# Performance work log

Measured on AMD Instinct MI355X. Metric: run time of the kernel, lower is better.

Reference implementation:

```python
import jax, jax.numpy as jnp
import numpy as np

N, F_IN, HID, OUT, K, L = 16000, 16, 256, 128, 8, 3


def setup_inputs() -> dict:
    key = jax.random.key(0)
    ks = jax.random.split(key, 8)
    rn = lambda k, sh, sc: (jax.random.normal(k, sh, jnp.float32) * sc)
    return {
        "x": rn(ks[0], (N, F_IN), 1.0),
        "coords": rn(ks[1], (N, 3), 1.0),
        "We": rn(ks[2], (F_IN, HID), 0.1),
        "be": jnp.zeros((HID,), jnp.float32),
        "gnn_W": rn(ks[3], (L, HID, HID), 0.05),
        "gnn_b": jnp.zeros((L, HID), jnp.float32),
        "Wp1": rn(ks[4], (HID, HID // 2), 0.05),
        "bp1": jnp.zeros((HID // 2,), jnp.float32),
        "Wp2": rn(ks[5], (HID // 2, OUT), 0.05),
        "bp2": jnp.zeros((OUT,), jnp.float32),
    }


def knn_edges(coords, k=K):
    # squared pairwise distances (same ordering as torch.cdist) -> kNN, drop self
    sq = jnp.sum(coords * coords, axis=1)
    d2 = sq[:, None] + sq[None, :] - 2.0 * (coords @ coords.T)  # [N, N]
    _, idx = jax.lax.top_k(-d2, k + 1)            # smallest k+1 (incl. self)
    nbr = idx[:, 1:]                               # [N, k]
    src = jnp.broadcast_to(jnp.arange(coords.shape[0])[:, None], nbr.shape)
    return src.reshape(-1), nbr.reshape(-1)       # edge_index rows


def gcn_layer(h, W, b, src, dst, n):
    # GCN with added self-loops and symmetric degree normalization
    deg = jnp.ones((n,), h.dtype).at[dst].add(1.0)   # in-degree + self-loop
    norm = jax.lax.rsqrt(deg)
    hw = h @ W                                        # [N, HID]
    msg = hw[src] * (norm[src] * norm[dst])[:, None]  # gather + scale
    agg = jax.ops.segment_sum(msg, dst, num_segments=n)
    agg = agg + hw * (norm * norm)[:, None]           # self-loop term
    return agg + b


def reference(x, coords, We, be, gnn_W, gnn_b, Wp1, bp1, Wp2, bp2):
    n = x.shape[0]
    src, dst = knn_edges(coords)
    h = x @ We + be                     # survey encoder -> [N, HID]
    for i in range(L):
        h = gcn_layer(h, gnn_W[i], gnn_b[i], src, dst, n)
        h = jax.nn.relu(h)              # dropout is identity in eval mode
    g = jnp.mean(h, axis=0)             # mean pooling (batch=None) -> [HID]
    out = jax.nn.relu(g @ Wp1 + bp1) @ Wp2 + bp2  # output projection -> [OUT]
    return out
```

## Files before the change

### kernel.cpp

```cpp
#include <hip/hip_runtime.h>
#include <math.h>

#define N_NODES 16000
#define F_IN    16
#define HID     256
#define OUTD    128
#define KNN     8
#define LAYERS  3
#define NEDGE   (N_NODES * KNN)

#define NPAD    16384
#define PARTS   4
#define PART_SZ (NPAD / PARTS)
#define SEGS    32
#define NMIN    (PARTS * SEGS)
#define CAPP    32
#define NZERO   32256

typedef __attribute__((ext_vector_type(8))) short  s8v;
typedef __attribute__((ext_vector_type(4))) float  f4v;

__device__ __forceinline__ unsigned short f2bf(float x) {
    unsigned u = __float_as_uint(x);
    unsigned r = u + 0x7fffu + ((u >> 16) & 1u);
    return (unsigned short)(r >> 16);
}
__device__ __forceinline__ float bf2f(unsigned short b) {
    return __uint_as_float(((unsigned)b) << 16);
}

__global__ __launch_bounds__(256) void prep_kernel(const float* __restrict__ coords,
                                                   float4* __restrict__ cand,
                                                   int* __restrict__ zero) {
    int i = blockIdx.x * 256 + threadIdx.x;
    int z = i * 2;
    if (z < NZERO) { zero[z] = 0; zero[z + 1] = 0; }
    if (i >= NPAD) return;
    if (i < N_NODES) {
        float x = coords[3 * i], y = coords[3 * i + 1], z2 = coords[3 * i + 2];
        cand[i] = make_float4(-2.f * x, -2.f * y, -2.f * z2, x * x + y * y + z2 * z2);
    } else {
        cand[i] = make_float4(0.f, 0.f, 0.f, INFINITY);
    }
}

#define DIST(qx, qy, qz, c) fmaf(qx, c.x, fmaf(qy, c.y, fmaf(qz, c.z, c.w)))

__global__ __launch_bounds__(256) void knn_min_kernel(const float* __restrict__ coords,
                                                      const float4* __restrict__ cand,
                                                      float* __restrict__ minv) {
    int tid  = threadIdx.x;
    int seg  = tid & 31;
    int qg   = tid >> 5;
    int qbase = blockIdx.x * 64;
    int part = blockIdx.y;

    float qx[8], qy[8], qz[8], m[8];
#pragma unroll
    for (int i = 0; i < 8; ++i) {
        int q = qbase + i * 8 + qg;
        qx[i] = coords[q * 3]; qy[i] = coords[q * 3 + 1]; qz[i] = coords[q * 3 + 2];
        m[i] = INFINITY;
    }

    int pbase = part * PART_SZ;
#pragma unroll 2
    for (int c0 = 0; c0 < PART_SZ; c0 += 128) {
        float4 v0 = cand[pbase + c0 + seg];
        float4 v1 = cand[pbase + c0 + seg + 32];
        float4 v2 = cand[pbase + c0 + seg + 64];
        float4 v3 = cand[pbase + c0 + seg + 96];
#pragma unroll
        for (int i = 0; i < 8; ++i) {
            float d0 = DIST(qx[i], qy[i], qz[i], v0);
            float d1 = DIST(qx[i], qy[i], qz[i], v1);
            float d2 = DIST(qx[i], qy[i], qz[i], v2);
            float d3 = DIST(qx[i], qy[i], qz[i], v3);
            m[i] = fminf(m[i], fminf(fminf(d0, d1), fminf(d2, d3)));
        }
    }
#pragma unroll
    for (int i = 0; i < 8; ++i) {
        int q = qbase + i * 8 + qg;
        minv[(q * PARTS + part) * SEGS + seg] = m[i];
    }
}

__global__ __launch_bounds__(256) void knn_collect_kernel(const float* __restrict__ coords,
                                                          const float4* __restrict__ cand,
                                                          const float* __restrict__ minv,
                                                          int* __restrict__ cnt,
                                                          float2* __restrict__ cl) {
    __shared__ int scnt[64];
    __shared__ float stau[64];
    int tid  = threadIdx.x;
    int seg  = tid & 31;
    int qg   = tid >> 5;
    int qbase = blockIdx.x * 64;
    int part  = blockIdx.y;

    if (tid < 64) {
        int q = qbase + tid;
        const float4* mv = (const float4*)(minv + (size_t)q * NMIN);
        float b[9];
#pragma unroll
        for (int p = 0; p < 9; ++p) b[p] = INFINITY;
#pragma unroll
        for (int c = 0; c < 16; ++c) {
            float4 a0 = mv[c * 2], a1 = mv[c * 2 + 1];
            float v = fminf(fminf(fminf(a0.x, a0.y), fminf(a0.z, a0.w)),
                            fminf(fminf(a1.x, a1.y), fminf(a1.z, a1.w)));
#pragma unroll
            for (int p = 8; p >= 1; --p) {
                bool  up = v < b[p - 1];
                b[p] = up ? b[p - 1] : (v < b[p] ? v : b[p]);
            }
            if (v < b[0]) b[0] = v;
        }
        stau[tid] = b[8];
        scnt[tid] = 0;
    }

    float qx[8], qy[8], qz[8], tt[8];
#pragma unroll
    for (int i = 0; i < 8; ++i) {
        int q = qbase + i * 8 + qg;
        qx[i] = coords[q * 3]; qy[i] = coords[q * 3 + 1]; qz[i] = coords[q * 3 + 2];
    }
    __syncthreads();
#pragma unroll
    for (int i = 0; i < 8; ++i) tt[i] = stau[i * 8 + qg];

    int pbase = part * PART_SZ;
    for (int c0 = 0; c0 < PART_SZ; c0 += 128) {
        float4 v0 = cand[pbase + c0 + seg];
        float4 v1 = cand[pbase + c0 + seg + 32];
        float4 v2 = cand[pbase + c0 + seg + 64];
        float4 v3 = cand[pbase + c0 + seg + 96];
        int jb = pbase + c0 + seg;
#pragma unroll
        for (int i = 0; i < 8; ++i) {
            float d0 = DIST(qx[i], qy[i], qz[i], v0);
            float d1 = DIST(qx[i], qy[i], qz[i], v1);
            float d2 = DIST(qx[i], qy[i], qz[i], v2);
            float d3 = DIST(qx[i], qy[i], qz[i], v3);
            float m4 = fminf(fminf(d0, d1), fminf(d2, d3));
            if (m4 <= tt[i]) {
                int qi = qbase + i * 8 + qg;
                int cb = (int)(((size_t)qi * PARTS + part) * CAPP);
                if (d0 <= tt[i]) {
                    int pos = atomicAdd(&scnt[i * 8 + qg], 1);
                    if (pos < CAPP) cl[cb + pos] = make_float2(d0, __int_as_float(jb));
                }
                if (d1 <= tt[i]) {
                    int pos = atomicAdd(&scnt[i * 8 + qg], 1);
                    if (pos < CAPP) cl[cb + pos] = make_float2(d1, __int_as_float(jb + 32));
                }
                if (d2 <= tt[i]) {
                    int pos = atomicAdd(&scnt[i * 8 + qg], 1);
                    if (pos < CAPP) cl[cb + pos] = make_float2(d2, __int_as_float(jb + 64));
                }
                if (d3 <= tt[i]) {
                    int pos = atomicAdd(&scnt[i * 8 + qg], 1);
                    if (pos < CAPP) cl[cb + pos] = make_float2(d3, __int_as_float(jb + 96));
                }
            }
        }
    }
    __syncthreads();
    if (tid < 64) cnt[(size_t)(qbase + tid) * PARTS + part] = scnt[tid];
}

#define INS9L(bd, bi, d, j)                                                   \
    {                                                                         \
        _Pragma("unroll")                                                     \
        for (int p = 8; p >= 1; --p) {                                        \
            bool up = (d) < bd[p-1] || ((d) == bd[p-1] && (j) < bi[p-1]);     \
            bool in = (d) < bd[p]   || ((d) == bd[p]   && (j) < bi[p]);       \
            float nd = up ? bd[p-1] : (in ? (d) : bd[p]);                     \
            int   ni = up ? bi[p-1] : (in ? (j) : bi[p]);                     \
            bd[p] = nd; bi[p] = ni;                                           \
        }                                                                     \
        if ((d) < bd[0] || ((d) == bd[0] && (j) < bi[0])) {                   \
            bd[0] = (d); bi[0] = (j);                                         \
        }                                                                     \
    }

__global__ __launch_bounds__(256) void knn_select_kernel(const float* __restrict__ coords,
                                                         const float4* __restrict__ cand,
                                                         const float2* __restrict__ cl,
                                                         const int* __restrict__ cnt,
                                                         int* __restrict__ nbr,
                                                         int* __restrict__ indeg) {
    int q = blockIdx.x * 256 + threadIdx.x;
    if (q >= N_NODES) return;
    float bd[9]; int bi[9];
#pragma unroll
    for (int p = 0; p < 9; ++p) { bd[p] = INFINITY; bi[p] = 0x7fffffff; }
    int n0 = cnt[(size_t)q * PARTS + 0];
    int n1 = cnt[(size_t)q * PARTS + 1];
    int n2 = cnt[(size_t)q * PARTS + 2];
    int n3 = cnt[(size_t)q * PARTS + 3];
    if (n0 <= CAPP && n1 <= CAPP && n2 <= CAPP && n3 <= CAPP) {
#pragma unroll
        for (int p = 0; p < PARTS; ++p) {
            int n = (p == 0) ? n0 : (p == 1) ? n1 : (p == 2) ? n2 : n3;
            const float2* segp = cl + ((size_t)q * PARTS + p) * CAPP;
            for (int i = 0; i < n; ++i) {
                float2 e = segp[i];
                float d = e.x; int j = __float_as_int(e.y);
                INS9L(bd, bi, d, j);
            }
        }
    } else {
        float qx = coords[q*3], qy = coords[q*3+1], qz = coords[q*3+2];
        for (int j = 0; j < NPAD; ++j) {
            float4 c = cand[j];
            float d = DIST(qx, qy, qz, c);
            if (d < bd[8] || (d == bd[8] && j < bi[8])) INS9L(bd, bi, d, j);
        }
    }
#pragma unroll
    for (int p = 1; p < 9; ++p) {
        nbr[q * 8 + p - 1] = bi[p];
        atomicAdd(&indeg[bi[p]], 1);
    }
}

__global__ __launch_bounds__(1024) void scan_kernel(const int* __restrict__ indeg,
                                                    int* __restrict__ offs,
                                                    float* __restrict__ norm) {
    __shared__ int ssum[1024];
    int t = threadIdx.x;
    const int CH = 16;
    int base = t * CH;
    int s = 0;
    for (int c = 0; c < CH; ++c) {
        int idx = base + c;
        if (idx < N_NODES) s += indeg[idx];
    }
    ssum[t] = s;
    __syncthreads();
    for (int d = 1; d < 1024; d <<= 1) {
        int v = (t >= d) ? ssum[t - d] : 0;
        __syncthreads();
        ssum[t] += v;
        __syncthreads();
    }
    int run = ssum[t] - s;
    for (int c = 0; c < CH; ++c) {
        int idx = base + c;
        if (idx < N_NODES) {
            int dg = indeg[idx];
            offs[idx] = run;
            run += dg;
            norm[idx] = rsqrtf((float)(1 + dg));
        }
    }
    if (t == 1023) offs[N_NODES] = ssum[1023];
}

__global__ void fill_kernel(const int* __restrict__ nbr, const int* __restrict__ offs,
                            int* __restrict__ cursor, int* __restrict__ adj) {
    int e = blockIdx.x * blockDim.x + threadIdx.x;
    if (e < NEDGE) {
        int d   = nbr[e];
        int src = e >> 3;
        int pos = atomicAdd(&cursor[d], 1);
        adj[offs[d] + pos] = src;
    }
}

__global__ __launch_bounds__(256) void gemm_kernel(const float* __restrict__ A,
                                                   const float* __restrict__ B,
                                                   float* __restrict__ C,
                                                   int K,
                                                   const float* __restrict__ bias,
                                                   const float* __restrict__ Wg,
                                                   unsigned short* __restrict__ WThi,
                                                   unsigned short* __restrict__ WTlo) {
    if (blockIdx.y == 4) {
        for (int idx = blockIdx.x * 256 + threadIdx.x; idx < LAYERS * 65536;
             idx += 64000) {
            int l = idx >> 16;
            int r = idx & 65535;
            int k = r >> 8, j = r & 255;
            float xv = Wg[idx];
            unsigned short hb = f2bf(xv);
            size_t o = (size_t)l * 65536 + j * 256 + k;
            WThi[o] = hb;
            WTlo[o] = f2bf(xv - bf2f(hb));
        }
        return;
    }
    __shared__ float As[16][68];
    __shared__ float Bs[16][64];
    int tid = threadIdx.x;
    int rowBase = blockIdx.x * 64;
    int colBase = blockIdx.y * 64;
    int rg = tid >> 4;
    int cg = tid & 15;

    int ar = tid >> 2;
    int ac = (tid & 3) * 4;
    int bk = tid >> 4;
    int bn = (tid & 15) * 4;

    float4 acc0 = {0,0,0,0}, acc1 = {0,0,0,0}, acc2 = {0,0,0,0}, acc3 = {0,0,0,0};

    for (int kb = 0; kb < K; kb += 16) {
        float4 av = *(const float4*)(A + (size_t)(rowBase + ar) * K + kb + ac);
        float4 bv = *(const float4*)(B + (size_t)(kb + bk) * HID + colBase + bn);
        __syncthreads();
        As[ac + 0][ar] = av.x; As[ac + 1][ar] = av.y;
        As[ac + 2][ar] = av.z; As[ac + 3][ar] = av.w;
        *(float4*)&Bs[bk][bn] = bv;
        __syncthreads();
#pragma unroll
        for (int k = 0; k < 16; ++k) {
            float4 a = *(const float4*)&As[k][rg * 4];
            float4 b = *(const float4*)&Bs[k][cg * 4];
            acc0.x = fmaf(a.x, b.x, acc0.x); acc0.y = fmaf(a.x, b.y, acc0.y);
            acc0.z = fmaf(a.x, b.z, acc0.z); acc0.w = fmaf(a.x, b.w, acc0.w);
            acc1.x = fmaf(a.y, b.x, acc1.x); acc1.y = fmaf(a.y, b.y, acc1.y);
            acc1.z = fmaf(a.y, b.z, acc1.z); acc1.w = fmaf(a.y, b.w, acc1.w);
            acc2.x = fmaf(a.z, b.x, acc2.x); acc2.y = fmaf(a.z, b.y, acc2.y);
            acc2.z = fmaf(a.z, b.z, acc2.z); acc2.w = fmaf(a.z, b.w, acc2.w);
            acc3.x = fmaf(a.w, b.x, acc3.x); acc3.y = fmaf(a.w, b.y, acc3.y);
            acc3.z = fmaf(a.w, b.z, acc3.z); acc3.w = fmaf(a.w, b.w, acc3.w);
        }
        __syncthreads();
    }

    int row = rowBase + rg * 4;
    int col = colBase + cg * 4;
    float4 bb = *(const float4*)(bias + col);

    float4 v;
    v.x = acc0.x + bb.x; v.y = acc0.y + bb.y; v.z = acc0.z + bb.z; v.w = acc0.w + bb.w;
    *(float4*)(C + (size_t)(row + 0) * HID + col) = v;
    v.x = acc1.x + bb.x; v.y = acc1.y + bb.y; v.z = acc1.z + bb.z; v.w = acc1.w + bb.w;
    *(float4*)(C + (size_t)(row + 1) * HID + col) = v;
    v.x = acc2.x + bb.x; v.y = acc2.y + bb.y; v.z = acc2.z + bb.z; v.w = acc2.w + bb.w;
    *(float4*)(C + (size_t)(row + 2) * HID + col) = v;
    v.x = acc3.x + bb.x; v.y = acc3.y + bb.y; v.z = acc3.z + bb.z; v.w = acc3.w + bb.w;
    *(float4*)(C + (size_t)(row + 3) * HID + col) = v;
}

__global__ __launch_bounds__(256) void mfma_gemm_kernel(const float* __restrict__ A,
                                                        const unsigned short* __restrict__ WThi,
                                                        const unsigned short* __restrict__ WTlo,
                                                        unsigned short* __restrict__ C,
                                                        const float* __restrict__ rowscale) {
    __shared__ unsigned short Ahi[64][40], Alo[64][40];
    __shared__ unsigned short Bhi[64][40], Blo[64][40];
    int tid = threadIdx.x;
    int rowBase = blockIdx.x * 64;
    int colBase = blockIdx.y * 64;
    int wave = tid >> 6;
    int lane = tid & 63;
    int fr = lane & 15;
    int fg = lane >> 4;

    int asr = tid >> 2;
    int ask = (tid & 3) * 8;
    int bsj = tid >> 2;
    int bsk = (tid & 3) * 8;

    f4v acc[4];
#pragma unroll
    for (int c = 0; c < 4; ++c) acc[c] = (f4v){0.f, 0.f, 0.f, 0.f};

    for (int kb = 0; kb < HID; kb += 32) {
        const float4* ap = (const float4*)(A + (size_t)(rowBase + asr) * HID + kb + ask);
        float4 a0 = ap[0], a1 = ap[1];
        uint4 bh0 = *(const uint4*)(WThi + (size_t)(colBase + bsj) * HID + kb + bsk);
        uint4 bl0 = *(const uint4*)(WTlo + (size_t)(colBase + bsj) * HID + kb + bsk);

        __syncthreads();
        {
            float xv[8] = {a0.x, a0.y, a0.z, a0.w, a1.x, a1.y, a1.z, a1.w};
            s8v hv, lv;
#pragma unroll
            for (int e = 0; e < 8; ++e) {
                unsigned short hb = f2bf(xv[e]);
                float hf = bf2f(hb);
                hv[e] = (short)hb;
                lv[e] = (short)f2bf(xv[e] - hf);
            }
            *(s8v*)&Ahi[asr][ask] = hv;
            *(s8v*)&Alo[asr][ask] = lv;
        }
        *(uint4*)&Bhi[bsj][bsk] = bh0;
        *(uint4*)&Blo[bsj][bsk] = bl0;
        __syncthreads();

        s8v afh = *(s8v*)&Ahi[wave * 16 + fr][fg * 8];
        s8v afl = *(s8v*)&Alo[wave * 16 + fr][fg * 8];
#pragma unroll
        for (int c = 0; c < 4; ++c) {
            s8v bfh = *(s8v*)&Bhi[c * 16 + fr][fg * 8];
            s8v bfl = *(s8v*)&Blo[c * 16 + fr][fg * 8];
            acc[c] = __builtin_amdgcn_mfma_f32_16x16x32_bf16(afh, bfh, acc[c], 0, 0, 0);
            acc[c] = __builtin_amdgcn_mfma_f32_16x16x32_bf16(afh, bfl, acc[c], 0, 0, 0);
            acc[c] = __builtin_amdgcn_mfma_f32_16x16x32_bf16(afl, bfh, acc[c], 0, 0, 0);
        }
    }

    float sc[4];
#pragma unroll
    for (int r = 0; r < 4; ++r) sc[r] = rowscale[rowBase + wave * 16 + fg * 4 + r];
#pragma unroll
    for (int c = 0; c < 4; ++c) {
        int col = colBase + c * 16 + fr;
#pragma unroll
        for (int r = 0; r < 4; ++r) {
            int row = rowBase + wave * 16 + fg * 4 + r;
            C[(size_t)row * HID + col] = f2bf(acc[c][r] * sc[r]);
        }
    }
}

__global__ __launch_bounds__(256) void agg_kernel(const unsigned short* __restrict__ u,
                                                  const float* __restrict__ norm,
                                                  const float* __restrict__ bias,
                                                  const int* __restrict__ offs,
                                                  const int* __restrict__ adj,
                                                  float* __restrict__ hout) {
    int node = blockIdx.x * 4 + (threadIdx.x >> 6);
    int lane = threadIdx.x & 63;
    const ushort4* up = (const ushort4*)u;
    ushort4 sv = up[(size_t)node * 64 + lane];
    float ax = bf2f(sv.x), ay = bf2f(sv.y), az = bf2f(sv.z), aw = bf2f(sv.w);
    int e0 = offs[node], e1 = offs[node + 1];
    for (int e = e0; e < e1; ++e) {
        int s = adj[e];
        ushort4 v = up[(size_t)s * 64 + lane];
        ax += bf2f(v.x); ay += bf2f(v.y); az += bf2f(v.z); aw += bf2f(v.w);
    }
    float nm = norm[node];
    float4 bb = ((const float4*)bias)[lane];
    float4 r;
    r.x = fmaxf(fmaf(nm, ax, bb.x), 0.0f);
    r.y = fmaxf(fmaf(nm, ay, bb.y), 0.0f);
    r.z = fmaxf(fmaf(nm, az, bb.z), 0.0f);
    r.w = fmaxf(fmaf(nm, aw, bb.w), 0.0f);
    ((float4*)hout)[(size_t)node * 64 + lane] = r;
}

__global__ __launch_bounds__(256) void pool_kernel(const float* __restrict__ h,
                                                   float* __restrict__ gsum) {
    int t = threadIdx.x;
    float acc = 0.f;
    int start = blockIdx.x * 250;
    for (int i = 0; i < 250; ++i) acc += h[(size_t)(start + i) * HID + t];
    atomicAdd(&gsum[t], acc);
}

__global__ __launch_bounds__(128) void head_kernel(const float* __restrict__ gsum,
                                                   const float* __restrict__ Wp1,
                                                   const float* __restrict__ bp1,
                                                   const float* __restrict__ Wp2,
                                                   const float* __restrict__ bp2,
                                                   float* __restrict__ out) {
    __shared__ float gl[256];
    __shared__ float hid[128];
    int t = threadIdx.x;
    const float inv = 1.0f / 16000.0f;
    gl[t]       = gsum[t]       * inv;
    gl[t + 128] = gsum[t + 128] * inv;
    __syncthreads();
    float a = bp1[t];
    for (int k = 0; k < 256; ++k) a = fmaf(gl[k], Wp1[k * 128 + t], a);
    hid[t] = fmaxf(a, 0.0f);
    __syncthreads();
    float o = bp2[t];
    for (int k = 0; k < 128; ++k) o = fmaf(hid[k], Wp2[k * 128 + t], o);
    out[t] = o;
}

extern "C" void kernel_launch(void* const* d_in, const int* in_sizes, int n_in,
                              void* d_out, int out_size, void* d_ws, size_t ws_size,
                              hipStream_t stream) {
    const float* x      = (const float*)d_in[0];
    const float* coords = (const float*)d_in[1];
    const float* We     = (const float*)d_in[2];
    const float* be     = (const float*)d_in[3];
    const float* gnn_W  = (const float*)d_in[4];
    const float* gnn_b  = (const float*)d_in[5];
    const float* Wp1    = (const float*)d_in[6];
    const float* bp1    = (const float*)d_in[7];
    const float* Wp2    = (const float*)d_in[8];
    const float* bp2    = (const float*)d_in[9];
    float* out = (float*)d_out;

    char* ws = (char*)d_ws;
    float* h     = (float*)(ws + 0);
    char*  ureg  = ws + 16384000;
    int*   nbr   = (int*)  (ws + 32768000);
    int*   adj   = (int*)  (ws + 33280000);
    int*   indeg = (int*)  (ws + 33792000);
    int*   cursor= (int*)  (ws + 33856000);
    float* gsum  = (float*)(ws + 33920000);
    int*   offs  = (int*)  (ws + 33921024);
    float* norm  = (float*)(ws + 33985152);
    float4* cand = (float4*)(ws + 34049280);

    unsigned short* u16 = (unsigned short*)ureg;
    float*  minv = (float*)ureg;
    int*    cnt  = (int*)  (ureg + 8256000);
    unsigned short* WThi = (unsigned short*)(ureg + 8512000);
    unsigned short* WTlo = (unsigned short*)(ureg + 8905216);
    float2* cl   = (float2*)h;

    prep_kernel<<<NPAD / 256, 256, 0, stream>>>(coords, cand, indeg);
    knn_min_kernel<<<dim3(N_NODES / 64, PARTS), 256, 0, stream>>>(coords, cand, minv);
    knn_collect_kernel<<<dim3(N_NODES / 64, PARTS), 256, 0, stream>>>(coords, cand, minv, cnt, cl);
    knn_select_kernel<<<(N_NODES + 255) / 256, 256, 0, stream>>>(coords, cand, cl, cnt, nbr, indeg);

    scan_kernel<<<1, 1024, 0, stream>>>(indeg, offs, norm);
    fill_kernel<<<(NEDGE + 255) / 256, 256, 0, stream>>>(nbr, offs, cursor, adj);

    gemm_kernel<<<dim3(N_NODES / 64, 5), 256, 0, stream>>>(x, We, h, F_IN, be,
                                                           gnn_W, WThi, WTlo);
    for (int l = 0; l < LAYERS; ++l) {
        mfma_gemm_kernel<<<dim3(N_NODES / 64, 4), 256, 0, stream>>>(
            h, WThi + (size_t)l * 65536, WTlo + (size_t)l * 65536, u16, norm);
        agg_kernel<<<N_NODES / 4, 256, 0, stream>>>(u16, norm, gnn_b + (size_t)l * HID,
                                                    offs, adj, h);
    }
    pool_kernel<<<64, 256, 0, stream>>>(h, gsum);
    head_kernel<<<1, 128, 0, stream>>>(gsum, Wp1, bp1, Wp2, bp2, out);
}
```

Before: 287.4 us.

## Store activations in bf16, drop A split-precision MFMA, fuse pooling, split tau kernel

Activations h are now stored as bf16 instead of fp32, so the MFMA GEMM loads bf16 directly and drops the hi/lo split of A. That leaves two MFMAs per tile instead of three, and GEMM input and agg output traffic are halved. Mean pooling is fused into the last aggregation layer through shared-memory atomics and 64 partial sums, which removes pool_kernel. The per-query tau computation moves out of the collect kernel into its own tau_kernel, and the kNN min pass now scans only half of each partition. These changes trade accuracy (bf16 activations, a looser tau bound from a partial min scan that raises the collect workload) for less memory traffic and fewer MFMAs.

```diff
diff --git a/kernel.cpp b/kernel.cpp
--- a/kernel.cpp
+++ b/kernel.cpp
@@ -12,10 +12,10 @@
 #define NPAD    16384
 #define PARTS   4
 #define PART_SZ (NPAD / PARTS)
+#define HALF_SZ 2048
 #define SEGS    32
 #define NMIN    (PARTS * SEGS)
 #define CAPP    32
-#define NZERO   32256
 
 typedef __attribute__((ext_vector_type(8))) short  s8v;
 typedef __attribute__((ext_vector_type(4))) float  f4v;
@@ -31,10 +31,12 @@
 
 __global__ __launch_bounds__(256) void prep_kernel(const float* __restrict__ coords,
                                                    float4* __restrict__ cand,
-                                                   int* __restrict__ zero) {
+                                                   int4* __restrict__ zeroA,
+                                                   int4* __restrict__ zeroB) {
     int i = blockIdx.x * 256 + threadIdx.x;
-    int z = i * 2;
-    if (z < NZERO) { zero[z] = 0; zero[z + 1] = 0; }
+    int4 z4 = {0, 0, 0, 0};
+    if (i < 8000) zeroA[i] = z4;
+    if (i < 4096) zeroB[i] = z4;
     if (i >= NPAD) return;
     if (i < N_NODES) {
         float x = coords[3 * i], y = coords[3 * i + 1], z2 = coords[3 * i + 2];
@@ -65,7 +67,7 @@
 
     int pbase = part * PART_SZ;
 #pragma unroll 2
-    for (int c0 = 0; c0 < PART_SZ; c0 += 128) {
+    for (int c0 = 0; c0 < HALF_SZ; c0 += 128) {
         float4 v0 = cand[pbase + c0 + seg];
         float4 v1 = cand[pbase + c0 + seg + 32];
         float4 v2 = cand[pbase + c0 + seg + 64];
@@ -86,50 +88,50 @@
     }
 }
 
+__global__ __launch_bounds__(256) void tau_kernel(const float* __restrict__ minv,
+                                                  float* __restrict__ tau) {
+    int q = blockIdx.x * 256 + threadIdx.x;
+    if (q >= N_NODES) return;
+    float b[9];
+#pragma unroll
+    for (int p = 0; p < 9; ++p) b[p] = INFINITY;
+    const float4* mv = (const float4*)(minv + (size_t)q * NMIN);
+#pragma unroll
+    for (int c = 0; c < 16; ++c) {
+        float4 a0 = mv[c * 2], a1 = mv[c * 2 + 1];
+        float v = fminf(fminf(fminf(a0.x, a0.y), fminf(a0.z, a0.w)),
+                        fminf(fminf(a1.x, a1.y), fminf(a1.z, a1.w)));
+#pragma unroll
+        for (int p = 8; p >= 1; --p) {
+            bool  up = v < b[p - 1];
+            b[p] = up ? b[p - 1] : (v < b[p] ? v : b[p]);
+        }
+        if (v < b[0]) b[0] = v;
+    }
+    tau[q] = b[8];
+}
+
 __global__ __launch_bounds__(256) void knn_collect_kernel(const float* __restrict__ coords,
                                                           const float4* __restrict__ cand,
-                                                          const float* __restrict__ minv,
+                                                          const float* __restrict__ tau,
                                                           int* __restrict__ cnt,
                                                           float2* __restrict__ cl) {
     __shared__ int scnt[64];
-    __shared__ float stau[64];
     int tid  = threadIdx.x;
     int seg  = tid & 31;
     int qg   = tid >> 5;
     int qbase = blockIdx.x * 64;
     int part  = blockIdx.y;
 
-    if (tid < 64) {
-        int q = qbase + tid;
-        const float4* mv = (const float4*)(minv + (size_t)q * NMIN);
-        float b[9];
-#pragma unroll
-        for (int p = 0; p < 9; ++p) b[p] = INFINITY;
-#pragma unroll
-        for (int c = 0; c < 16; ++c) {
-            float4 a0 = mv[c * 2], a1 = mv[c * 2 + 1];
-            float v = fminf(fminf(fminf(a0.x, a0.y), fminf(a0.z, a0.w)),
-                            fminf(fminf(a1.x, a1.y), fminf(a1.z, a1.w)));
-#pragma unroll
-            for (int p = 8; p >= 1; --p) {
-                bool  up = v < b[p - 1];
-                b[p] = up ? b[p - 1] : (v < b[p] ? v : b[p]);
-            }
-            if (v < b[0]) b[0] = v;
-        }
-        stau[tid] = b[8];
-        scnt[tid] = 0;
-    }
-
     float qx[8], qy[8], qz[8], tt[8];
 #pragma unroll
     for (int i = 0; i < 8; ++i) {
         int q = qbase + i * 8 + qg;
         qx[i] = coords[q * 3]; qy[i] = coords[q * 3 + 1]; qz[i] = coords[q * 3 + 2];
-    }
+        tt[i] = tau[q];
+    }
+    if (tid < 64) scnt[tid] = 0;
     __syncthreads();
-#pragma unroll
-    for (int i = 0; i < 8; ++i) tt[i] = stau[i * 8 + qg];
 
     int pbase = part * PART_SZ;
     for (int c0 = 0; c0 < PART_SZ; c0 += 128) {
@@ -273,7 +275,7 @@
 
 __global__ __launch_bounds__(256) void gemm_kernel(const float* __restrict__ A,
                                                    const float* __restrict__ B,
-                                                   float* __restrict__ C,
+                                                   unsigned short* __restrict__ C,
                                                    int K,
                                                    const float* __restrict__ bias,
                                                    const float* __restrict__ Wg,
@@ -336,24 +338,28 @@
     int col = colBase + cg * 4;
     float4 bb = *(const float4*)(bias + col);
 
-    float4 v;
-    v.x = acc0.x + bb.x; v.y = acc0.y + bb.y; v.z = acc0.z + bb.z; v.w = acc0.w + bb.w;
-    *(float4*)(C + (size_t)(row + 0) * HID + col) = v;
-    v.x = acc1.x + bb.x; v.y = acc1.y + bb.y; v.z = acc1.z + bb.z; v.w = acc1.w + bb.w;
-    *(float4*)(C + (size_t)(row + 1) * HID + col) = v;
-    v.x = acc2.x + bb.x; v.y = acc2.y + bb.y; v.z = acc2.z + bb.z; v.w = acc2.w + bb.w;
-    *(float4*)(C + (size_t)(row + 2) * HID + col) = v;
-    v.x = acc3.x + bb.x; v.y = acc3.y + bb.y; v.z = acc3.z + bb.z; v.w = acc3.w + bb.w;
-    *(float4*)(C + (size_t)(row + 3) * HID + col) = v;
-}
-
-__global__ __launch_bounds__(256) void mfma_gemm_kernel(const float* __restrict__ A,
+    ushort4 o;
+    o.x = f2bf(acc0.x + bb.x); o.y = f2bf(acc0.y + bb.y);
+    o.z = f2bf(acc0.z + bb.z); o.w = f2bf(acc0.w + bb.w);
+    *(ushort4*)(C + (size_t)(row + 0) * HID + col) = o;
+    o.x = f2bf(acc1.x + bb.x); o.y = f2bf(acc1.y + bb.y);
+    o.z = f2bf(acc1.z + bb.z); o.w = f2bf(acc1.w + bb.w);
+    *(ushort4*)(C + (size_t)(row + 1) * HID + col) = o;
+    o.x = f2bf(acc2.x + bb.x); o.y = f2bf(acc2.y + bb.y);
+    o.z = f2bf(acc2.z + bb.z); o.w = f2bf(acc2.w + bb.w);
+    *(ushort4*)(C + (size_t)(row + 2) * HID + col) = o;
+    o.x = f2bf(acc3.x + bb.x); o.y = f2bf(acc3.y + bb.y);
+    o.z = f2bf(acc3.z + bb.z); o.w = f2bf(acc3.w + bb.w);
+    *(ushort4*)(C + (size_t)(row + 3) * HID + col) = o;
+}
+
+__global__ __launch_bounds__(256) void mfma_gemm_kernel(const unsigned short* __restrict__ A,
                                                         const unsigned short* __restrict__ WThi,
                                                         const unsigned short* __restrict__ WTlo,
                                                         unsigned short* __restrict__ C,
                                                         const float* __restrict__ rowscale) {
-    __shared__ unsigned short Ahi[64][40], Alo[64][40];
-    __shared__ unsigned short Bhi[64][40], Blo[64][40];
+    __shared__ unsigned short Ah[64][40];
+    __shared__ unsigned short Bh[64][40], Bl[64][40];
     int tid = threadIdx.x;
     int rowBase = blockIdx.x * 64;
     int colBase = blockIdx.y * 64;
@@ -364,46 +370,28 @@
 
     int asr = tid >> 2;
     int ask = (tid & 3) * 8;
-    int bsj = tid >> 2;
-    int bsk = (tid & 3) * 8;
 
     f4v acc[4];
 #pragma unroll
     for (int c = 0; c < 4; ++c) acc[c] = (f4v){0.f, 0.f, 0.f, 0.f};
 
     for (int kb = 0; kb < HID; kb += 32) {
-        const float4* ap = (const float4*)(A + (size_t)(rowBase + asr) * HID + kb + ask);
-        float4 a0 = ap[0], a1 = ap[1];
-        uint4 bh0 = *(const uint4*)(WThi + (size_t)(colBase + bsj) * HID + kb + bsk);
-        uint4 bl0 = *(const uint4*)(WTlo + (size_t)(colBase + bsj) * HID + kb + bsk);
-
-        __syncthreads();
-        {
-            float xv[8] = {a0.x, a0.y, a0.z, a0.w, a1.x, a1.y, a1.z, a1.w};
-            s8v hv, lv;
-#pragma unroll
-            for (int e = 0; e < 8; ++e) {
-                unsigned short hb = f2bf(xv[e]);
-                float hf = bf2f(hb);
-                hv[e] = (short)hb;
-                lv[e] = (short)f2bf(xv[e] - hf);
-            }
-            *(s8v*)&Ahi[asr][ask] = hv;
-            *(s8v*)&Alo[asr][ask] = lv;
-        }
-        *(uint4*)&Bhi[bsj][bsk] = bh0;
-        *(uint4*)&Blo[bsj][bsk] = bl0;
-        __syncthreads();
-
-        s8v afh = *(s8v*)&Ahi[wave * 16 + fr][fg * 8];
-        s8v afl = *(s8v*)&Alo[wave * 16 + fr][fg * 8];
+        uint4 av = *(const uint4*)(A    + (size_t)(rowBase + asr) * HID + kb + ask);
+        uint4 bh = *(const uint4*)(WThi + (size_t)(colBase + asr) * HID + kb + ask);
+        uint4 bl = *(const uint4*)(WTlo + (size_t)(colBase + asr) * HID + kb + ask);
+        __syncthreads();
+        *(uint4*)&Ah[asr][ask] = av;
+        *(uint4*)&Bh[asr][ask] = bh;
+        *(uint4*)&Bl[asr][ask] = bl;
+        __syncthreads();
+
+        s8v af = *(s8v*)&Ah[wave * 16 + fr][fg * 8];
 #pragma unroll
         for (int c = 0; c < 4; ++c) {
-            s8v bfh = *(s8v*)&Bhi[c * 16 + fr][fg * 8];
-            s8v bfl = *(s8v*)&Blo[c * 16 + fr][fg * 8];
-            acc[c] = __builtin_amdgcn_mfma_f32_16x16x32_bf16(afh, bfh, acc[c], 0, 0, 0);
-            acc[c] = __builtin_amdgcn_mfma_f32_16x16x32_bf16(afh, bfl, acc[c], 0, 0, 0);
-            acc[c] = __builtin_amdgcn_mfma_f32_16x16x32_bf16(afl, bfh, acc[c], 0, 0, 0);
+            s8v bfh = *(s8v*)&Bh[c * 16 + fr][fg * 8];
+            s8v bfl = *(s8v*)&Bl[c * 16 + fr][fg * 8];
+            acc[c] = __builtin_amdgcn_mfma_f32_16x16x32_bf16(af, bfh, acc[c], 0, 0, 0);
+            acc[c] = __builtin_amdgcn_mfma_f32_16x16x32_bf16(af, bfl, acc[c], 0, 0, 0);
         }
     }
 
@@ -426,9 +414,12 @@
                                                   const float* __restrict__ bias,
                                                   const int* __restrict__ offs,
                                                   const int* __restrict__ adj,
-                                                  float* __restrict__ hout) {
-    int node = blockIdx.x * 4 + (threadIdx.x >> 6);
-    int lane = threadIdx.x & 63;
+                                                  unsigned short* __restrict__ hout,
+                                                  float* __restrict__ gsumP) {
+    __shared__ float sacc[256];
+    int tid  = threadIdx.x;
+    int node = blockIdx.x * 4 + (tid >> 6);
+    int lane = tid & 63;
     const ushort4* up = (const ushort4*)u;
     ushort4 sv = up[(size_t)node * 64 + lane];
     float ax = bf2f(sv.x), ay = bf2f(sv.y), az = bf2f(sv.z), aw = bf2f(sv.w);
@@ -445,19 +436,23 @@
     r.y = fmaxf(fmaf(nm, ay, bb.y), 0.0f);
     r.z = fmaxf(fmaf(nm, az, bb.z), 0.0f);
     r.w = fmaxf(fmaf(nm, aw, bb.w), 0.0f);
-    ((float4*)hout)[(size_t)node * 64 + lane] = r;
-}
-
-__global__ __launch_bounds__(256) void pool_kernel(const float* __restrict__ h,
-                                                   float* __restrict__ gsum) {
-    int t = threadIdx.x;
-    float acc = 0.f;
-    int start = blockIdx.x * 250;
-    for (int i = 0; i < 250; ++i) acc += h[(size_t)(start + i) * HID + t];
-    atomicAdd(&gsum[t], acc);
-}
-
-__global__ __launch_bounds__(128) void head_kernel(const float* __restrict__ gsum,
+    ushort4 o;
+    o.x = f2bf(r.x); o.y = f2bf(r.y); o.z = f2bf(r.z); o.w = f2bf(r.w);
+    ((ushort4*)hout)[(size_t)node * 64 + lane] = o;
+
+    if (gsumP) {
+        sacc[tid] = 0.0f;
+        __syncthreads();
+        atomicAdd(&sacc[lane * 4 + 0], r.x);
+        atomicAdd(&sacc[lane * 4 + 1], r.y);
+        atomicAdd(&sacc[lane * 4 + 2], r.z);
+        atomicAdd(&sacc[lane * 4 + 3], r.w);
+        __syncthreads();
+        atomicAdd(&gsumP[(blockIdx.x & 63) * 256 + tid], sacc[tid]);
+    }
+}
+
+__global__ __launch_bounds__(128) void head_kernel(const float* __restrict__ gsumP,
                                                    const float* __restrict__ Wp1,
                                                    const float* __restrict__ bp1,
                                                    const float* __restrict__ Wp2,
@@ -467,8 +462,13 @@
     __shared__ float hid[128];
     int t = threadIdx.x;
     const float inv = 1.0f / 16000.0f;
-    gl[t]       = gsum[t]       * inv;
-    gl[t + 128] = gsum[t + 128] * inv;
+    float s0 = 0.f, s1 = 0.f;
+    for (int p = 0; p < 64; ++p) {
+        s0 += gsumP[p * 256 + t];
+        s1 += gsumP[p * 256 + t + 128];
+    }
+    gl[t]       = s0 * inv;
+    gl[t + 128] = s1 * inv;
     __syncthreads();
     float a = bp1[t];
     for (int k = 0; k < 256; ++k) a = fmaf(gl[k], Wp1[k * 128 + t], a);
@@ -495,27 +495,29 @@
     float* out = (float*)d_out;
 
     char* ws = (char*)d_ws;
-    float* h     = (float*)(ws + 0);
+    unsigned short* h = (unsigned short*)(ws + 0);
     char*  ureg  = ws + 16384000;
     int*   nbr   = (int*)  (ws + 32768000);
     int*   adj   = (int*)  (ws + 33280000);
     int*   indeg = (int*)  (ws + 33792000);
     int*   cursor= (int*)  (ws + 33856000);
-    float* gsum  = (float*)(ws + 33920000);
     int*   offs  = (int*)  (ws + 33921024);
     float* norm  = (float*)(ws + 33985152);
     float4* cand = (float4*)(ws + 34049280);
 
     unsigned short* u16 = (unsigned short*)ureg;
     float*  minv = (float*)ureg;
+    float*  tau  = (float*)(ureg + 8192000);
     int*    cnt  = (int*)  (ureg + 8256000);
     unsigned short* WThi = (unsigned short*)(ureg + 8512000);
     unsigned short* WTlo = (unsigned short*)(ureg + 8905216);
-    float2* cl   = (float2*)h;
-
-    prep_kernel<<<NPAD / 256, 256, 0, stream>>>(coords, cand, indeg);
+    float*  gsumP = (float*)(ureg + 9298432);
+    float2* cl   = (float2*)(ws + 0);
+
+    prep_kernel<<<NPAD / 256, 256, 0, stream>>>(coords, cand, (int4*)indeg, (int4*)gsumP);
     knn_min_kernel<<<dim3(N_NODES / 64, PARTS), 256, 0, stream>>>(coords, cand, minv);
-    knn_collect_kernel<<<dim3(N_NODES / 64, PARTS), 256, 0, stream>>>(coords, cand, minv, cnt, cl);
+    tau_kernel<<<(N_NODES + 255) / 256, 256, 0, stream>>>(minv, tau);
+    knn_collect_kernel<<<dim3(N_NODES / 64, PARTS), 256, 0, stream>>>(coords, cand, tau, cnt, cl);
     knn_select_kernel<<<(N_NODES + 255) / 256, 256, 0, stream>>>(coords, cand, cl, cnt, nbr, indeg);
 
     scan_kernel<<<1, 1024, 0, stream>>>(indeg, offs, norm);
@@ -527,8 +529,8 @@
         mfma_gemm_kernel<<<dim3(N_NODES / 64, 4), 256, 0, stream>>>(
             h, WThi + (size_t)l * 65536, WTlo + (size_t)l * 65536, u16, norm);
         agg_kernel<<<N_NODES / 4, 256, 0, stream>>>(u16, norm, gnn_b + (size_t)l * HID,
-                                                    offs, adj, h);
-    }
-    pool_kernel<<<64, 256, 0, stream>>>(h, gsum);
-    head_kernel<<<1, 128, 0, stream>>>(gsum, Wp1, bp1, Wp2, bp2, out);
-}
+                                                    offs, adj, h,
+                                                    (l == LAYERS - 1) ? gsumP : nullptr);
+    }
+    head_kernel<<<1, 128, 0, stream>>>(gsumP, Wp1, bp1, Wp2, bp2, out);
+}
```

Result: slower. 300.4 us (+4.5%).
